# Kernel optimization log

Hardware: AMD Instinct MI355X
Metric: run time of the kernel (lower is better)

The kernel has to match this reference:

```python
import jax, jax.numpy as jnp
import numpy as np

N_HASHES = 8
Q_ATTN = 128   # q_cluster_size == q_attn_size
K_ATTN = 128   # k_cluster_size == k_attn_size
LSH_R = 1.0


def setup_inputs() -> dict:
    key = jax.random.key(0)
    kq, kk, kv = jax.random.split(key, 3)
    B, Nq, Nk, D, Dv = 4, 8192, 8192, 64, 64
    return {
        "queries": jax.random.normal(kq, (B, Nq, D), dtype=jnp.float32),
        "keys":    jax.random.normal(kk, (B, Nk, D), dtype=jnp.float32),
        "values":  jax.random.normal(kv, (B, Nk, Dv), dtype=jnp.float32),
    }


def _cluster_positions(queries, keys):
    """XBOX+ asymmetric transform + E2LSH bucketing (torch.no_grad block).
    Returns q_positions (H,B,Nq), k_positions (H,B,Nk): per-hash permutations
    sorting tokens so that consecutive blocks of Q_ATTN/K_ATTN form clusters."""
    q = jax.lax.stop_gradient(queries)
    k = jax.lax.stop_gradient(keys)
    qn = jnp.linalg.norm(q, axis=-1, keepdims=True)          # (B,Nq,1)
    kn = jnp.linalg.norm(k, axis=-1, keepdims=True)          # (B,Nk,1)
    M2 = jnp.max(qn, axis=1, keepdims=True) ** 2 + jnp.max(kn, axis=1, keepdims=True) ** 2
    # Q(x)=[x, sqrt(M^2-|x|^2), 0], K(x)=[x, 0, sqrt(M^2-|x|^2)]
    Q = jnp.concatenate([q, jnp.sqrt(jnp.maximum(M2 - qn ** 2, 0.0)), jnp.zeros_like(qn)], axis=-1)
    K = jnp.concatenate([k, jnp.zeros_like(kn), jnp.sqrt(jnp.maximum(M2 - kn ** 2, 0.0))], axis=-1)
    De = Q.shape[-1]
    rk = jax.random.key(42)
    alpha = jax.random.normal(jax.random.fold_in(rk, 0), (N_HASHES, De), dtype=Q.dtype)
    beta = jax.random.uniform(jax.random.fold_in(rk, 1), (N_HASHES, 1, 1), dtype=Q.dtype,
                              minval=0.0, maxval=LSH_R)
    # E2LSH bucket id per token, one independent hash per round (same hash fn for q and k)
    qb = jnp.floor((jnp.einsum('bnd,hd->hbn', Q, alpha) + beta) / LSH_R)
    kb = jnp.floor((jnp.einsum('bnd,hd->hbn', K, alpha) + beta) / LSH_R)
    return jnp.argsort(qb, axis=-1), jnp.argsort(kb, axis=-1)


def _gather_seq(x, pos, H):
    # x: (B,N,D), pos: (H,B,N) -> (H,B,N,D) gathered along seq axis
    B, N, D = x.shape
    xr = jnp.broadcast_to(x[None], (H, B, N, D))
    idx = jnp.broadcast_to(pos[..., None], (H, B, N, D))
    return jnp.take_along_axis(xr, idx, axis=2)


def reference(queries, keys, values):
    B, Nq, D = queries.shape
    Nk = keys.shape[1]
    Dv = values.shape[-1]
    H = N_HASHES
    C = Nq // Q_ATTN  # num clusters (== Nk // K_ATTN)

    q_pos, k_pos = _cluster_positions(queries, keys)          # (H,B,Nq), (H,B,Nk)
    q_rev = jnp.argsort(q_pos, axis=-1)                       # inverse permutation

    sq = _gather_seq(queries, q_pos, H).reshape(H, B, C, Q_ATTN, D)
    sk = _gather_seq(keys,    k_pos, H).reshape(H, B, C, K_ATTN, D)
    sv = _gather_seq(values,  k_pos, H).reshape(H, B, C, K_ATTN, Dv)

    inner = jnp.einsum('hbcqd,hbckd->hbcqk', sq, sk)          # per-cluster scores (no 1/sqrt(d) scale, as in source)
    lse = jax.nn.logsumexp(inner, axis=-1, keepdims=True)     # (H,B,C,Qa,1)
    dots = jnp.exp(inner - lse)
    bo = jnp.einsum('hbcqk,hbckv->hbcqv', dots, sv).reshape(H, B, Nq, Dv)

    # scatter back to original order via inverse permutation
    o = jnp.take_along_axis(bo, jnp.broadcast_to(q_rev[..., None], (H, B, Nq, Dv)), axis=2)
    logits = jnp.take_along_axis(lse.reshape(H, B, Nq), q_rev, axis=2)
    probs = jax.nn.softmax(logits, axis=0)                    # combine n_hashes rounds by logsumexp weights
    return jnp.sum(o * probs[..., None], axis=0)              # (B,Nq,Dv)
```

## Files before the change

kernel.cpp:

```cpp
#include <hip/hip_runtime.h>
#include <stdint.h>

typedef unsigned int u32;
typedef unsigned long long u64;

#define BATCH 4
#define NSEQ  8192
#define DIM   64
#define NH    8
#define CSZ   128
#define NCLU  64

#define WS_ALPHA   0
#define WS_BETA    528
#define WS_MAXB    536
#define WS_QN      1024
#define WS_KEYS_B  266240
#define WS_LSE_B   2363392
#define WS_BO_B    3411968

typedef short bf16x8 __attribute__((ext_vector_type(8)));
typedef float f32x4 __attribute__((ext_vector_type(4)));
#define MFMA16(a, b, c) __builtin_amdgcn_mfma_f32_16x16x32_bf16(a, b, c, 0, 0, 0)

__device__ __forceinline__ u32 cvtpk(float lo, float hi) {
  u32 d;
  asm("v_cvt_pk_bf16_f32 %0, %1, %2" : "=v"(d) : "v"(lo), "v"(hi));
  return d;
}
__device__ __forceinline__ float uaf(u32 x) { return __uint_as_float(x); }

__device__ __forceinline__ void tf2x32(u32 k0, u32 k1, u32 x0, u32 x1, u32& o0, u32& o1) {
  u32 ks2 = k0 ^ k1 ^ 0x1BD11BDAu;
  x0 += k0; x1 += k1;
#define TF_RND(r) { x0 += x1; x1 = (x1 << (r)) | (x1 >> (32 - (r))); x1 ^= x0; }
  TF_RND(13) TF_RND(15) TF_RND(26) TF_RND(6)
  x0 += k1; x1 += ks2 + 1u;
  TF_RND(17) TF_RND(29) TF_RND(16) TF_RND(24)
  x0 += ks2; x1 += k0 + 2u;
  TF_RND(13) TF_RND(15) TF_RND(26) TF_RND(6)
  x0 += k0; x1 += k1 + 3u;
  TF_RND(17) TF_RND(29) TF_RND(16) TF_RND(24)
  x0 += k1; x1 += ks2 + 4u;
  TF_RND(13) TF_RND(15) TF_RND(26) TF_RND(6)
  x0 += ks2; x1 += k0 + 5u;
#undef TF_RND
  o0 = x0; o1 = x1;
}

__device__ __forceinline__ float bits01(u32 b) {
  return __uint_as_float((b >> 9) | 0x3f800000u) - 1.0f;
}

__device__ __forceinline__ float xla_erfinv(float x) {
  float x2 = __fmul_rn(x, x);
  float w = (float)(-log1p(-(double)x2));
  float p;
  if (w < 5.0f) {
    float ww = __fsub_rn(w, 2.5f);
    p = 2.81022636e-08f;
    p = __fadd_rn(3.43273939e-07f, __fmul_rn(p, ww));
    p = __fadd_rn(-3.5233877e-06f, __fmul_rn(p, ww));
    p = __fadd_rn(-4.39150654e-06f, __fmul_rn(p, ww));
    p = __fadd_rn(0.00021858087f, __fmul_rn(p, ww));
    p = __fadd_rn(-0.00125372503f, __fmul_rn(p, ww));
    p = __fadd_rn(-0.00417768164f, __fmul_rn(p, ww));
    p = __fadd_rn(0.246640727f, __fmul_rn(p, ww));
    p = __fadd_rn(1.50140941f, __fmul_rn(p, ww));
  } else {
    float ww = __fsub_rn(__fsqrt_rn(w), 3.0f);
    p = -0.000200214257f;
    p = __fadd_rn(0.000100950558f, __fmul_rn(p, ww));
    p = __fadd_rn(0.00134934322f, __fmul_rn(p, ww));
    p = __fadd_rn(-0.00367342844f, __fmul_rn(p, ww));
    p = __fadd_rn(0.00573950773f, __fmul_rn(p, ww));
    p = __fadd_rn(-0.0076224613f, __fmul_rn(p, ww));
    p = __fadd_rn(0.00943887047f, __fmul_rn(p, ww));
    p = __fadd_rn(1.00167406f, __fmul_rn(p, ww));
    p = __fadd_rn(2.83297682f, __fmul_rn(p, ww));
  }
  return __fmul_rn(p, x);
}

__global__ __launch_bounds__(256) void smyrf_rng(float* ws) {
  int t = threadIdx.x;
  float* alpha = ws + WS_ALPHA;
  float* beta  = ws + WS_BETA;
  u32*   maxb  = (u32*)(ws + WS_MAXB);
  if (t < 8) maxb[t] = 0u;
  u32 ka0, ka1, kb0, kb1;
  tf2x32(0u, 42u, 0u, 0u, ka0, ka1);
  tf2x32(0u, 42u, 0u, 1u, kb0, kb1);
  const float LO = __uint_as_float(0xBF7FFFFFu);
  const float SQ2 = 1.4142135623730951f;
  for (int i = t; i < 528; i += 256) {
    u32 o0, o1; tf2x32(ka0, ka1, 0u, (u32)i, o0, o1);
    u32 bits = o0 ^ o1;
    float u = __fadd_rn(__fmul_rn(bits01(bits), 2.0f), LO);
    alpha[i] = __fmul_rn(SQ2, xla_erfinv(u));
  }
  if (t < 8) {
    u32 o0, o1; tf2x32(kb0, kb1, 0u, (u32)t, o0, o1);
    beta[t] = bits01(o0 ^ o1);
  }
}

__global__ __launch_bounds__(256) void smyrf_norms(const float* __restrict__ Q,
                                                   const float* __restrict__ Kk,
                                                   float* ws) {
  int tid = blockIdx.x * 256 + threadIdx.x;
  int tensor = tid >> 15;
  const float* x = (tensor ? Kk : Q) + (size_t)(tid & 32767) * DIM;
  const float4* x4 = (const float4*)x;
  double s = 0.0;
  #pragma unroll
  for (int i = 0; i < 16; ++i) {
    float4 v = x4[i];
    s += (double)v.x * v.x + (double)v.y * v.y + (double)v.z * v.z + (double)v.w * v.w;
  }
  float qn = (float)sqrt(s);
  (ws + WS_QN)[tid] = qn;
  float wmax = qn;
  #pragma unroll
  for (int off = 1; off < 64; off <<= 1) wmax = fmaxf(wmax, __shfl_xor(wmax, off));
  __shared__ float red[4];
  int wave = threadIdx.x >> 6;
  if ((threadIdx.x & 63) == 0) red[wave] = wmax;
  __syncthreads();
  if (threadIdx.x == 0) {
    float m = fmaxf(fmaxf(red[0], red[1]), fmaxf(red[2], red[3]));
    int b = (tid >> 13) & 3;
    atomicMax((u32*)(ws + WS_MAXB) + tensor * 4 + b, __float_as_uint(m));
  }
}

__global__ __launch_bounds__(256) void smyrf_keys(const float* __restrict__ Q,
                                                  const float* __restrict__ Kk,
                                                  float* ws) {
  int tid = blockIdx.x * 256 + threadIdx.x;
  int tensor = tid >> 15;
  int b = (tid >> 13) & 3;
  int n = tid & 8191;
  const float* x = (tensor ? Kk : Q) + (size_t)(tid & 32767) * DIM;
  float r[64];
  const float4* x4 = (const float4*)x;
  #pragma unroll
  for (int i = 0; i < 16; ++i) {
    float4 v = x4[i];
    r[4 * i] = v.x; r[4 * i + 1] = v.y; r[4 * i + 2] = v.z; r[4 * i + 3] = v.w;
  }
  const float* alpha = ws + WS_ALPHA;
  const float* beta  = ws + WS_BETA;
  const u32*   maxb  = (const u32*)(ws + WS_MAXB);
  float qn = (ws + WS_QN)[tid];
  float mq = __uint_as_float(maxb[b]);
  float mk = __uint_as_float(maxb[4 + b]);
  float M2 = __fadd_rn(__fmul_rn(mq, mq), __fmul_rn(mk, mk));
  float ex = __fsqrt_rn(fmaxf(__fsub_rn(M2, __fmul_rn(qn, qn)), 0.0f));
  u32* keys = (u32*)((char*)ws + WS_KEYS_B);
  #pragma unroll 1
  for (int hh = 0; hh < NH; ++hh) {
    const float* al = alpha + hh * 66;
    double dot = 0.0;
    #pragma unroll
    for (int d = 0; d < 64; ++d) dot = fma((double)r[d], (double)al[d], dot);
    dot = fma((double)ex, (double)al[64 + tensor], dot);
    float val = __fadd_rn((float)dot, beta[hh]);
    float fb = floorf(val);
    int ib = (fb >= 262143.f) ? 262143 : ((fb <= -262144.f) ? -262144 : (int)fb);
    keys[((size_t)tensor * NH * BATCH + (size_t)hh * BATCH + b) * NSEQ + n] =
        ((u32)(ib + 262144) << 13) | (u32)n;
  }
}

__global__ __launch_bounds__(1024) void smyrf_sort(float* ws) {
  __shared__ u32 arrA[8192];
  __shared__ u32 arrB[8192];
  __shared__ u32 hist[16][256];
  __shared__ u32 scanbuf[256];
  __shared__ u32 wmn[16], wmx[16], mnmx[2];
  u32* base = (u32*)((char*)ws + WS_KEYS_B) + (size_t)blockIdx.x * 8192;
  int t = threadIdx.x;
  int w = t >> 6, l = t & 63;
  u64 ltmask = (1ull << l) - 1ull;

  u32 mn = 0xFFFFFFFFu, mx = 0u;
  for (int i = t; i < 8192; i += 1024) {
    u32 k = base[i];
    arrA[i] = k;
    u32 bk = k >> 13;
    mn = min(mn, bk); mx = max(mx, bk);
  }
  #pragma unroll
  for (int off = 1; off < 64; off <<= 1) {
    mn = min(mn, (u32)__shfl_xor((int)mn, off));
    mx = max(mx, (u32)__shfl_xor((int)mx, off));
  }
  if (l == 0) { wmn[w] = mn; wmx[w] = mx; }
  __syncthreads();
  if (t == 0) {
    u32 a = wmn[0], bb = wmx[0];
    #pragma unroll
    for (int i = 1; i < 16; ++i) { a = min(a, wmn[i]); bb = max(bb, wmx[i]); }
    mnmx[0] = a; mnmx[1] = bb;
  }
  __syncthreads();
  u32 minb = mnmx[0];
  u32 range = mnmx[1] - minb;
  int npass = (range < 256u) ? 1 : ((range < 65536u) ? 2 : 3);

  u32* src = arrA;
  u32* dst = arrB;
  for (int p = 0; p < npass; ++p) {
    int sh = 8 * p;
    for (int i = t; i < 16 * 256; i += 1024) ((u32*)hist)[i] = 0u;
    __syncthreads();
    #pragma unroll 1
    for (int r = 0; r < 8; ++r) {
      u32 key = src[w * 512 + r * 64 + l];
      u32 d = (((key >> 13) - minb) >> sh) & 255u;
      atomicAdd(&hist[w][d], 1u);
    }
    __syncthreads();
    u32 mytot = 0;
    if (t < 256) {
      u32 run = 0;
      #pragma unroll
      for (int ww = 0; ww < 16; ++ww) { u32 c = hist[ww][t]; hist[ww][t] = run; run += c; }
      mytot = run;
      scanbuf[t] = run;
    }
    __syncthreads();
    for (int s = 1; s < 256; s <<= 1) {
      u32 v = 0;
      if (t < 256 && t >= s) v = scanbuf[t - s];
      __syncthreads();
      if (t < 256) scanbuf[t] += v;
      __syncthreads();
    }
    if (t < 256) {
      u32 off = scanbuf[t] - mytot;
      #pragma unroll
      for (int ww = 0; ww < 16; ++ww) hist[ww][t] += off;
    }
    __syncthreads();
    #pragma unroll 1
    for (int r = 0; r < 8; ++r) {
      u32 key = src[w * 512 + r * 64 + l];
      u32 d = (((key >> 13) - minb) >> sh) & 255u;
      u64 peers = ~0ull;
      #pragma unroll
      for (int bit = 0; bit < 8; ++bit) {
        bool myb = (d >> bit) & 1u;
        u64 vote = __ballot(myb);
        peers &= myb ? vote : ~vote;
      }
      u32 rank = (u32)__popcll(peers & ltmask);
      u32 cnt = (u32)__popcll(peers);
      int leaderLane = (int)__ffsll((long long)peers) - 1;
      u32 old = 0;
      if (l == leaderLane) old = atomicAdd(&hist[w][d], cnt);
      old = (u32)__shfl((int)old, leaderLane);
      dst[old + rank] = key;
    }
    __syncthreads();
    u32* tmp = src; src = dst; dst = tmp;
  }
  for (int i = t; i < 8192; i += 1024) base[i] = src[i];
}

__device__ __forceinline__ int swz(int row, int kb) { return row * 128 + (kb ^ ((row & 7) << 4)); }

__global__ __launch_bounds__(256) void smyrf_attn_mfma(const float* __restrict__ Q,
                                                       const float* __restrict__ K,
                                                       const float* __restrict__ V,
                                                       float* __restrict__ ws) {
  __shared__ uint4 smem_u4[4096];
  char* sm = (char*)smem_u4;
  int id = blockIdx.x;
  int c = id & 63, b = (id >> 6) & 3, h = id >> 8;
  int t = threadIdx.x;
  int lane = t & 63, w = t >> 6;
  int cl = lane & 15, ag = lane >> 4;

  const u32* keys = (const u32*)((const char*)ws + WS_KEYS_B);
  const u32* qkp = keys + ((size_t)h * BATCH + b) * NSEQ + c * CSZ;
  const u32* kkp = keys + (size_t)NH * BATCH * NSEQ + ((size_t)h * BATCH + b) * NSEQ + c * CSZ;
  const float* Qb = Q + (size_t)b * NSEQ * DIM;
  const float* Kb = K + (size_t)b * NSEQ * DIM;
  const float* Vb = V + (size_t)b * NSEQ * DIM;

  {
    int row = t & 127;
    int tensor = t >> 7;
    int tok = (int)((tensor ? kkp[row] : qkp[row]) & 8191);
    const float* src = (tensor ? Kb : Qb) + (size_t)tok * DIM;
    char* hb = sm + tensor * 32768;
    char* lb = hb + 16384;
    int sw = (row & 7) << 4;
    #pragma unroll
    for (int c8 = 0; c8 < 8; ++c8) {
      float4 a = *(const float4*)(src + c8 * 8);
      float4 cc = *(const float4*)(src + c8 * 8 + 4);
      float v[8] = {a.x, a.y, a.z, a.w, cc.x, cc.y, cc.z, cc.w};
      uint4 hv, lv;
      u32 hx;
      hx = cvtpk(v[0], v[1]); hv.x = hx;
      lv.x = cvtpk(v[0] - uaf(hx << 16), v[1] - uaf(hx & 0xFFFF0000u));
      hx = cvtpk(v[2], v[3]); hv.y = hx;
      lv.y = cvtpk(v[2] - uaf(hx << 16), v[3] - uaf(hx & 0xFFFF0000u));
      hx = cvtpk(v[4], v[5]); hv.z = hx;
      lv.z = cvtpk(v[4] - uaf(hx << 16), v[5] - uaf(hx & 0xFFFF0000u));
      hx = cvtpk(v[6], v[7]); hv.w = hx;
      lv.w = cvtpk(v[6] - uaf(hx << 16), v[7] - uaf(hx & 0xFFFF0000u));
      int off = row * 128 + ((c8 * 16) ^ sw);
      *(uint4*)&hb[off] = hv;
      *(uint4*)&lb[off] = lv;
    }
  }
  __syncthreads();

  f32x4 S[2][8];
  #pragma unroll
  for (int m = 0; m < 2; ++m)
    #pragma unroll
    for (int n = 0; n < 8; ++n) S[m][n] = (f32x4){0.f, 0.f, 0.f, 0.f};
  {
    const char* Qhi = sm, *Qlo = sm + 16384, *Khi = sm + 32768, *Klo = sm + 49152;
    #pragma unroll
    for (int kk_ = 0; kk_ < 2; ++kk_) {
      int kb = kk_ * 64 + ag * 16;
      bf16x8 qh0 = *(const bf16x8*)&Qhi[swz(w * 32 + cl, kb)];
      bf16x8 qh1 = *(const bf16x8*)&Qhi[swz(w * 32 + 16 + cl, kb)];
      bf16x8 ql0 = *(const bf16x8*)&Qlo[swz(w * 32 + cl, kb)];
      bf16x8 ql1 = *(const bf16x8*)&Qlo[swz(w * 32 + 16 + cl, kb)];
      #pragma unroll
      for (int n = 0; n < 8; ++n) {
        int o = swz(n * 16 + cl, kb);
        bf16x8 kh = *(const bf16x8*)&Khi[o];
        bf16x8 kl = *(const bf16x8*)&Klo[o];
        S[0][n] = MFMA16(qh0, kh, S[0][n]);
        S[1][n] = MFMA16(qh1, kh, S[1][n]);
        S[0][n] = MFMA16(qh0, kl, S[0][n]);
        S[1][n] = MFMA16(qh1, kl, S[1][n]);
        S[0][n] = MFMA16(ql0, kh, S[0][n]);
        S[1][n] = MFMA16(ql1, kh, S[1][n]);
      }
    }
  }

  float inv_[2][4];
  float* lse = (float*)((char*)ws + WS_LSE_B);
  #pragma unroll
  for (int m = 0; m < 2; ++m)
    #pragma unroll
    for (int r = 0; r < 4; ++r) {
      float mx = S[m][0][r];
      #pragma unroll
      for (int n = 1; n < 8; ++n) mx = fmaxf(mx, S[m][n][r]);
      mx = fmaxf(mx, __shfl_xor(mx, 1));
      mx = fmaxf(mx, __shfl_xor(mx, 2));
      mx = fmaxf(mx, __shfl_xor(mx, 4));
      mx = fmaxf(mx, __shfl_xor(mx, 8));
      float sum = 0.f;
      #pragma unroll
      for (int n = 0; n < 8; ++n) { float e = __expf(S[m][n][r] - mx); S[m][n][r] = e; sum += e; }
      sum += __shfl_xor(sum, 1);
      sum += __shfl_xor(sum, 2);
      sum += __shfl_xor(sum, 4);
      sum += __shfl_xor(sum, 8);
      inv_[m][r] = 1.0f / sum;
      if (cl == 0) {
        int q = w * 32 + m * 16 + ag * 4 + r;
        lse[(((size_t)h * BATCH + b) << 13) + (qkp[q] & 8191)] = mx + __logf(sum);
      }
    }

  f32x4 O[4][2];
  #pragma unroll
  for (int mt = 0; mt < 4; ++mt)
    #pragma unroll
    for (int nt = 0; nt < 2; ++nt) O[mt][nt] = (f32x4){0.f, 0.f, 0.f, 0.f};

  #pragma unroll
  for (int half = 0; half < 2; ++half) {
    __syncthreads();
    #pragma unroll
    for (int m = 0; m < 2; ++m)
      #pragma unroll
      for (int r = 0; r < 4; ++r) {
        int row = w * 32 + m * 16 + ag * 4 + r;
        int sw2 = (row & 7) << 4;
        float iv = inv_[m][r];
        float p0 = S[m][half * 4 + 0][r] * iv;
        float p1 = S[m][half * 4 + 1][r] * iv;
        float p2 = S[m][half * 4 + 2][r] * iv;
        float p3 = S[m][half * 4 + 3][r] * iv;
        u32 h01 = cvtpk(p0, p1), h23 = cvtpk(p2, p3);
        u32 e01 = cvtpk(p0 - uaf(h01 << 16), p1 - uaf(h01 & 0xFFFF0000u));
        u32 e23 = cvtpk(p2 - uaf(h23 << 16), p3 - uaf(h23 & 0xFFFF0000u));
        int base = row * 128;
        int o0 = base + ((2 * (0 * 16 + cl)) ^ sw2);
        int o1 = base + ((2 * (1 * 16 + cl)) ^ sw2);
        int o2 = base + ((2 * (2 * 16 + cl)) ^ sw2);
        int o3 = base + ((2 * (3 * 16 + cl)) ^ sw2);
        *(ushort*)&sm[o0] = (ushort)h01;         *(ushort*)&sm[16384 + o0] = (ushort)e01;
        *(ushort*)&sm[o1] = (ushort)(h01 >> 16); *(ushort*)&sm[16384 + o1] = (ushort)(e01 >> 16);
        *(ushort*)&sm[o2] = (ushort)h23;         *(ushort*)&sm[16384 + o2] = (ushort)e23;
        *(ushort*)&sm[o3] = (ushort)(h23 >> 16); *(ushort*)&sm[16384 + o3] = (ushort)(e23 >> 16);
      }
    if (half == 0) {
      int tok = t >> 1, dh = (t & 1) * 32;
      const float* vs = Vb + (size_t)(kkp[tok] & 8191) * DIM + dh;
      #pragma unroll
      for (int c4 = 0; c4 < 8; ++c4) {
        float4 a = *(const float4*)(vs + c4 * 4);
        u32 h01 = cvtpk(a.x, a.y), h23 = cvtpk(a.z, a.w);
        u32 e01 = cvtpk(a.x - uaf(h01 << 16), a.y - uaf(h01 & 0xFFFF0000u));
        u32 e23 = cvtpk(a.z - uaf(h23 << 16), a.w - uaf(h23 & 0xFFFF0000u));
        u32 hhv[4] = {h01 & 0xFFFFu, h01 >> 16, h23 & 0xFFFFu, h23 >> 16};
        u32 llv[4] = {e01 & 0xFFFFu, e01 >> 16, e23 & 0xFFFFu, e23 >> 16};
        #pragma unroll
        for (int j = 0; j < 4; ++j) {
          int dv = dh + c4 * 4 + j;
          int off = dv * 256 + ((2 * tok) ^ ((dv & 7) << 5));
          *(ushort*)&sm[32768 + off] = (ushort)hhv[j];
          *(ushort*)&sm[49152 + off] = (ushort)llv[j];
        }
      }
    }
    __syncthreads();
    #pragma unroll
    for (int k2 = 0; k2 < 2; ++k2) {
      int kbP = k2 * 64 + ag * 16;
      int kbV = half * 128 + k2 * 64 + ag * 16;
      bf16x8 p0h = *(const bf16x8*)&sm[swz(w * 32 + cl, kbP)];
      bf16x8 p0l = *(const bf16x8*)&sm[16384 + swz(w * 32 + cl, kbP)];
      bf16x8 p1h = *(const bf16x8*)&sm[swz(w * 32 + 16 + cl, kbP)];
      bf16x8 p1l = *(const bf16x8*)&sm[16384 + swz(w * 32 + 16 + cl, kbP)];
      #pragma unroll
      for (int mt = 0; mt < 4; ++mt) {
        int dv = mt * 16 + cl;
        int off = dv * 256 + (kbV ^ ((dv & 7) << 5));
        bf16x8 vh = *(const bf16x8*)&sm[32768 + off];
        bf16x8 vl = *(const bf16x8*)&sm[49152 + off];
        O[mt][0] = MFMA16(vh, p0h, O[mt][0]);
        O[mt][0] = MFMA16(vh, p0l, O[mt][0]);
        O[mt][0] = MFMA16(vl, p0h, O[mt][0]);
        O[mt][1] = MFMA16(vh, p1h, O[mt][1]);
        O[mt][1] = MFMA16(vh, p1l, O[mt][1]);
        O[mt][1] = MFMA16(vl, p1h, O[mt][1]);
      }
    }
  }

  ushort* bo = (ushort*)((char*)ws + WS_BO_B);
  #pragma unroll
  for (int nt = 0; nt < 2; ++nt) {
    int q = w * 32 + nt * 16 + cl;
    int tok = (int)(qkp[q] & 8191);
    ushort* orow = bo + ((((size_t)h * BATCH + b) << 13) + tok) * 64;
    #pragma unroll
    for (int mt = 0; mt < 4; ++mt) {
      uint2 d2;
      d2.x = cvtpk(O[mt][nt][0], O[mt][nt][1]);
      d2.y = cvtpk(O[mt][nt][2], O[mt][nt][3]);
      *(uint2*)&orow[mt * 16 + ag * 4] = d2;
    }
  }
}

__global__ __launch_bounds__(256) void smyrf_combine(const float* __restrict__ ws,
                                                     float* __restrict__ out) {
  int tid = blockIdx.x * 256 + threadIdx.x;
  int f4i = tid & 15;
  int n = (tid >> 4) & 8191;
  int b = tid >> 17;
  const float* lse = (const float*)((const char*)ws + WS_LSE_B);
  const ushort* bo = (const ushort*)((const char*)ws + WS_BO_B);
  float l[8];
  #pragma unroll
  for (int hh = 0; hh < 8; ++hh) l[hh] = lse[(((size_t)hh * BATCH + b) << 13) + n];
  float m = l[0];
  #pragma unroll
  for (int hh = 1; hh < 8; ++hh) m = fmaxf(m, l[hh]);
  float w[8]; float sum = 0.0f;
  #pragma unroll
  for (int hh = 0; hh < 8; ++hh) { w[hh] = __expf(l[hh] - m); sum += w[hh]; }
  float inv = 1.0f / sum;
  float4 a; a.x = a.y = a.z = a.w = 0.0f;
  #pragma unroll
  for (int hh = 0; hh < 8; ++hh) {
    const ushort* p = bo + ((((size_t)hh * BATCH + b) << 13) + n) * 64 + f4i * 4;
    uint2 dd = *(const uint2*)p;
    float ww = w[hh] * inv;
    a.x = fmaf(ww, uaf(dd.x << 16), a.x);
    a.y = fmaf(ww, uaf(dd.x & 0xFFFF0000u), a.y);
    a.z = fmaf(ww, uaf(dd.y << 16), a.z);
    a.w = fmaf(ww, uaf(dd.y & 0xFFFF0000u), a.w);
  }
  ((float4*)out)[tid] = a;
}

extern "C" void kernel_launch(void* const* d_in, const int* in_sizes, int n_in,
                              void* d_out, int out_size, void* d_ws, size_t ws_size,
                              hipStream_t stream) {
  const float* q = (const float*)d_in[0];
  const float* k = (const float*)d_in[1];
  const float* v = (const float*)d_in[2];
  float* out = (float*)d_out;
  float* ws = (float*)d_ws;

  smyrf_rng<<<1, 256, 0, stream>>>(ws);
  smyrf_norms<<<256, 256, 0, stream>>>(q, k, ws);
  smyrf_keys<<<256, 256, 0, stream>>>(q, k, ws);
  smyrf_sort<<<64, 1024, 0, stream>>>(ws);
  smyrf_attn_mfma<<<NH * BATCH * NCLU, 256, 0, stream>>>(q, k, v, ws);
  smyrf_combine<<<2048, 256, 0, stream>>>(ws, out);
}
```

Baseline: 184.5 us.

## Keep Q fragments in registers and shrink LDS to fit three blocks per CU

Q rows are now loaded straight from global memory into per-lane bf16 hi/lo MFMA fragments instead of being staged through shared memory. That frees the Q half of LDS, so the block needs 48KB instead of 64KB and launch bounds ask for 3 blocks per CU. V is staged in 64-token halves per pass with a smaller transposed layout. s_setprio is raised around the MFMA loops. The intent is higher occupancy to hide the gather latency, at the cost of uncoalesced direct Q loads and extra register pressure.

```diff
diff --git a/kernel.cpp b/kernel.cpp
--- a/kernel.cpp
+++ b/kernel.cpp
@@ -29,6 +29,21 @@
   return d;
 }
 __device__ __forceinline__ float uaf(u32 x) { return __uint_as_float(x); }
+
+__device__ __forceinline__ void split8(const float* p, bf16x8& hi, bf16x8& lo) {
+  float4 a = *(const float4*)p;
+  float4 b = *(const float4*)(p + 4);
+  u32 h0 = cvtpk(a.x, a.y), h1 = cvtpk(a.z, a.w);
+  u32 h2 = cvtpk(b.x, b.y), h3 = cvtpk(b.z, b.w);
+  u32 l0 = cvtpk(a.x - uaf(h0 << 16), a.y - uaf(h0 & 0xFFFF0000u));
+  u32 l1 = cvtpk(a.z - uaf(h1 << 16), a.w - uaf(h1 & 0xFFFF0000u));
+  u32 l2 = cvtpk(b.x - uaf(h2 << 16), b.y - uaf(h2 & 0xFFFF0000u));
+  u32 l3 = cvtpk(b.z - uaf(h3 << 16), b.w - uaf(h3 & 0xFFFF0000u));
+  union { u32 u[4]; bf16x8 v; } H, L;
+  H.u[0] = h0; H.u[1] = h1; H.u[2] = h2; H.u[3] = h3;
+  L.u[0] = l0; L.u[1] = l1; L.u[2] = l2; L.u[3] = l3;
+  hi = H.v; lo = L.v;
+}
 
 __device__ __forceinline__ void tf2x32(u32 k0, u32 k1, u32 x0, u32 x1, u32& o0, u32& o1) {
   u32 ks2 = k0 ^ k1 ^ 0x1BD11BDAu;
@@ -271,11 +286,11 @@
 
 __device__ __forceinline__ int swz(int row, int kb) { return row * 128 + (kb ^ ((row & 7) << 4)); }
 
-__global__ __launch_bounds__(256) void smyrf_attn_mfma(const float* __restrict__ Q,
-                                                       const float* __restrict__ K,
-                                                       const float* __restrict__ V,
-                                                       float* __restrict__ ws) {
-  __shared__ uint4 smem_u4[4096];
+__global__ __launch_bounds__(256, 3) void smyrf_attn_mfma(const float* __restrict__ Q,
+                                                          const float* __restrict__ K,
+                                                          const float* __restrict__ V,
+                                                          float* __restrict__ ws) {
+  __shared__ uint4 smem_u4[3072];
   char* sm = (char*)smem_u4;
   int id = blockIdx.x;
   int c = id & 63, b = (id >> 6) & 3, h = id >> 8;
@@ -290,32 +305,33 @@
   const float* Kb = K + (size_t)b * NSEQ * DIM;
   const float* Vb = V + (size_t)b * NSEQ * DIM;
 
+  bf16x8 qh[2][2], ql[2][2];
   {
-    int row = t & 127;
-    int tensor = t >> 7;
-    int tok = (int)((tensor ? kkp[row] : qkp[row]) & 8191);
-    const float* src = (tensor ? Kb : Qb) + (size_t)tok * DIM;
-    char* hb = sm + tensor * 32768;
-    char* lb = hb + 16384;
+    int tok0 = (int)(qkp[w * 32 + cl] & 8191);
+    int tok1 = (int)(qkp[w * 32 + 16 + cl] & 8191);
+    const float* s0 = Qb + (size_t)tok0 * DIM;
+    const float* s1 = Qb + (size_t)tok1 * DIM;
+    #pragma unroll
+    for (int kk_ = 0; kk_ < 2; ++kk_) {
+      int e = kk_ * 32 + ag * 8;
+      split8(s0 + e, qh[kk_][0], ql[kk_][0]);
+      split8(s1 + e, qh[kk_][1], ql[kk_][1]);
+    }
+  }
+
+  {
+    int row = t >> 1;
+    int eh = (t & 1) * 32;
+    int tok = (int)(kkp[row] & 8191);
+    const float* src = Kb + (size_t)tok * DIM + eh;
     int sw = (row & 7) << 4;
     #pragma unroll
-    for (int c8 = 0; c8 < 8; ++c8) {
-      float4 a = *(const float4*)(src + c8 * 8);
-      float4 cc = *(const float4*)(src + c8 * 8 + 4);
-      float v[8] = {a.x, a.y, a.z, a.w, cc.x, cc.y, cc.z, cc.w};
-      uint4 hv, lv;
-      u32 hx;
-      hx = cvtpk(v[0], v[1]); hv.x = hx;
-      lv.x = cvtpk(v[0] - uaf(hx << 16), v[1] - uaf(hx & 0xFFFF0000u));
-      hx = cvtpk(v[2], v[3]); hv.y = hx;
-      lv.y = cvtpk(v[2] - uaf(hx << 16), v[3] - uaf(hx & 0xFFFF0000u));
-      hx = cvtpk(v[4], v[5]); hv.z = hx;
-      lv.z = cvtpk(v[4] - uaf(hx << 16), v[5] - uaf(hx & 0xFFFF0000u));
-      hx = cvtpk(v[6], v[7]); hv.w = hx;
-      lv.w = cvtpk(v[6] - uaf(hx << 16), v[7] - uaf(hx & 0xFFFF0000u));
-      int off = row * 128 + ((c8 * 16) ^ sw);
-      *(uint4*)&hb[off] = hv;
-      *(uint4*)&lb[off] = lv;
+    for (int g = 0; g < 4; ++g) {
+      bf16x8 hi, lo;
+      split8(src + g * 8, hi, lo);
+      int off = row * 128 + (((eh + g * 8) * 2) ^ sw);
+      *(bf16x8*)&sm[off] = hi;
+      *(bf16x8*)&sm[16384 + off] = lo;
     }
   }
   __syncthreads();
@@ -326,27 +342,25 @@
     #pragma unroll
     for (int n = 0; n < 8; ++n) S[m][n] = (f32x4){0.f, 0.f, 0.f, 0.f};
   {
-    const char* Qhi = sm, *Qlo = sm + 16384, *Khi = sm + 32768, *Klo = sm + 49152;
+    const char* Khi = sm, *Klo = sm + 16384;
+    __builtin_amdgcn_s_setprio(1);
     #pragma unroll
     for (int kk_ = 0; kk_ < 2; ++kk_) {
       int kb = kk_ * 64 + ag * 16;
-      bf16x8 qh0 = *(const bf16x8*)&Qhi[swz(w * 32 + cl, kb)];
-      bf16x8 qh1 = *(const bf16x8*)&Qhi[swz(w * 32 + 16 + cl, kb)];
-      bf16x8 ql0 = *(const bf16x8*)&Qlo[swz(w * 32 + cl, kb)];
-      bf16x8 ql1 = *(const bf16x8*)&Qlo[swz(w * 32 + 16 + cl, kb)];
       #pragma unroll
       for (int n = 0; n < 8; ++n) {
         int o = swz(n * 16 + cl, kb);
         bf16x8 kh = *(const bf16x8*)&Khi[o];
         bf16x8 kl = *(const bf16x8*)&Klo[o];
-        S[0][n] = MFMA16(qh0, kh, S[0][n]);
-        S[1][n] = MFMA16(qh1, kh, S[1][n]);
-        S[0][n] = MFMA16(qh0, kl, S[0][n]);
-        S[1][n] = MFMA16(qh1, kl, S[1][n]);
-        S[0][n] = MFMA16(ql0, kh, S[0][n]);
-        S[1][n] = MFMA16(ql1, kh, S[1][n]);
+        S[0][n] = MFMA16(qh[kk_][0], kh, S[0][n]);
+        S[1][n] = MFMA16(qh[kk_][1], kh, S[1][n]);
+        S[0][n] = MFMA16(qh[kk_][0], kl, S[0][n]);
+        S[1][n] = MFMA16(qh[kk_][1], kl, S[1][n]);
+        S[0][n] = MFMA16(ql[kk_][0], kh, S[0][n]);
+        S[1][n] = MFMA16(ql[kk_][1], kh, S[1][n]);
       }
     }
+    __builtin_amdgcn_s_setprio(0);
   }
 
   float inv_[2][4];
@@ -409,41 +423,43 @@
         *(ushort*)&sm[o2] = (ushort)h23;         *(ushort*)&sm[16384 + o2] = (ushort)e23;
         *(ushort*)&sm[o3] = (ushort)(h23 >> 16); *(ushort*)&sm[16384 + o3] = (ushort)(e23 >> 16);
       }
-    if (half == 0) {
-      int tok = t >> 1, dh = (t & 1) * 32;
-      const float* vs = Vb + (size_t)(kkp[tok] & 8191) * DIM + dh;
-      #pragma unroll
-      for (int c4 = 0; c4 < 8; ++c4) {
-        float4 a = *(const float4*)(vs + c4 * 4);
+    {
+      int tokL = t >> 2;
+      int dh = (t & 3) * 16;
+      int tok = (int)(kkp[half * 64 + tokL] & 8191);
+      const float* vs = Vb + (size_t)tok * DIM + dh;
+      #pragma unroll
+      for (int g = 0; g < 4; ++g) {
+        float4 a = *(const float4*)(vs + g * 4);
         u32 h01 = cvtpk(a.x, a.y), h23 = cvtpk(a.z, a.w);
         u32 e01 = cvtpk(a.x - uaf(h01 << 16), a.y - uaf(h01 & 0xFFFF0000u));
         u32 e23 = cvtpk(a.z - uaf(h23 << 16), a.w - uaf(h23 & 0xFFFF0000u));
-        u32 hhv[4] = {h01 & 0xFFFFu, h01 >> 16, h23 & 0xFFFFu, h23 >> 16};
-        u32 llv[4] = {e01 & 0xFFFFu, e01 >> 16, e23 & 0xFFFFu, e23 >> 16};
+        u32 hv[4] = {h01 & 0xFFFFu, h01 >> 16, h23 & 0xFFFFu, h23 >> 16};
+        u32 lv[4] = {e01 & 0xFFFFu, e01 >> 16, e23 & 0xFFFFu, e23 >> 16};
         #pragma unroll
         for (int j = 0; j < 4; ++j) {
-          int dv = dh + c4 * 4 + j;
-          int off = dv * 256 + ((2 * tok) ^ ((dv & 7) << 5));
-          *(ushort*)&sm[32768 + off] = (ushort)hhv[j];
-          *(ushort*)&sm[49152 + off] = (ushort)llv[j];
+          int dv = dh + g * 4 + j;
+          int off = dv * 128 + ((2 * tokL) ^ ((dv & 7) << 4));
+          *(ushort*)&sm[32768 + off] = (ushort)hv[j];
+          *(ushort*)&sm[40960 + off] = (ushort)lv[j];
         }
       }
     }
     __syncthreads();
+    __builtin_amdgcn_s_setprio(1);
     #pragma unroll
     for (int k2 = 0; k2 < 2; ++k2) {
-      int kbP = k2 * 64 + ag * 16;
-      int kbV = half * 128 + k2 * 64 + ag * 16;
-      bf16x8 p0h = *(const bf16x8*)&sm[swz(w * 32 + cl, kbP)];
-      bf16x8 p0l = *(const bf16x8*)&sm[16384 + swz(w * 32 + cl, kbP)];
-      bf16x8 p1h = *(const bf16x8*)&sm[swz(w * 32 + 16 + cl, kbP)];
-      bf16x8 p1l = *(const bf16x8*)&sm[16384 + swz(w * 32 + 16 + cl, kbP)];
+      int kb = k2 * 64 + ag * 16;
+      bf16x8 p0h = *(const bf16x8*)&sm[swz(w * 32 + cl, kb)];
+      bf16x8 p0l = *(const bf16x8*)&sm[16384 + swz(w * 32 + cl, kb)];
+      bf16x8 p1h = *(const bf16x8*)&sm[swz(w * 32 + 16 + cl, kb)];
+      bf16x8 p1l = *(const bf16x8*)&sm[16384 + swz(w * 32 + 16 + cl, kb)];
       #pragma unroll
       for (int mt = 0; mt < 4; ++mt) {
         int dv = mt * 16 + cl;
-        int off = dv * 256 + (kbV ^ ((dv & 7) << 5));
+        int off = dv * 128 + (kb ^ ((dv & 7) << 4));
         bf16x8 vh = *(const bf16x8*)&sm[32768 + off];
-        bf16x8 vl = *(const bf16x8*)&sm[49152 + off];
+        bf16x8 vl = *(const bf16x8*)&sm[40960 + off];
         O[mt][0] = MFMA16(vh, p0h, O[mt][0]);
         O[mt][0] = MFMA16(vh, p0l, O[mt][0]);
         O[mt][0] = MFMA16(vl, p0h, O[mt][0]);
@@ -452,6 +468,7 @@
         O[mt][1] = MFMA16(vl, p1h, O[mt][1]);
       }
     }
+    __builtin_amdgcn_s_setprio(0);
   }
 
   ushort* bo = (ushort*)((char*)ws + WS_BO_B);
```

New measurement: 173.7 us. 1.06x faster.
